# Performance work log

Hardware: AMD Instinct MI355X
Metric: run time of the kernel (lower is better)

The kernel has to match this reference:

```python
import jax, jax.numpy as jnp
import numpy as np

N, E = 10000, 320000
NF, HF = 256, 256  # input_nf/output_nf, hidden_nf
EPS = 1e-8


def setup_inputs() -> dict:
    key = jax.random.key(0)
    ks = jax.random.split(key, 20)
    h = jax.random.normal(ks[0], (N, NF), jnp.float32)
    coord = jax.random.normal(ks[1], (N, 3), jnp.float32)
    edge_index = jax.random.randint(ks[2], (2, E), 0, N, jnp.int32)

    def dense(k, fan_in, fan_out, scale=None):
        s = scale if scale is not None else 1.0 / np.sqrt(fan_in)
        W = jax.random.normal(k, (fan_in, fan_out), jnp.float32) * s
        b = jnp.zeros((fan_out,), jnp.float32)
        return W, b

    We1, be1 = dense(ks[3], 2 * NF + 1, HF)   # edge_mlp layer 1
    We2, be2 = dense(ks[4], HF, HF)           # edge_mlp layer 2
    Wn1, bn1 = dense(ks[5], HF + NF, HF)      # node_mlp layer 1
    Wn2, bn2 = dense(ks[6], HF, NF)           # node_mlp layer 2
    Wc1, bc1 = dense(ks[7], HF, HF)           # coord_mlp layer 1
    Wc2, bc2 = dense(ks[8], HF, 1, scale=0.001)  # coord_mlp final, tiny init (xavier gain=0.001)
    return dict(h=h, coord=coord, edge_index=edge_index,
                We1=We1, be1=be1, We2=We2, be2=be2,
                Wn1=Wn1, bn1=bn1, Wn2=Wn2, bn2=bn2,
                Wc1=Wc1, bc1=bc1, Wc2=Wc2, bc2=bc2)


def _segment_sum(data, seg_ids, num_segments):
    return jax.ops.segment_sum(data, seg_ids, num_segments=num_segments)


def reference(h, coord, edge_index, We1, be1, We2, be2, Wn1, bn1, Wn2, bn2, Wc1, bc1, Wc2, bc2):
    row, col = edge_index[0], edge_index[1]

    # coord2radial
    coord_diff = coord[row] - coord[col]                    # [E, 3]
    radial = jnp.sum(coord_diff ** 2, axis=1, keepdims=True)  # [E, 1]

    # edge model: MLP on [h_i, h_j, ||x_i - x_j||^2]
    edge_in = jnp.concatenate([h[row], h[col], radial], axis=1)  # [E, 2*NF+1]
    e = jax.nn.silu(edge_in @ We1 + be1)
    edge_feat = jax.nn.silu(e @ We2 + be2)                  # [E, HF]

    # coord model: coord_diff * coord_mlp(edge_feat), mean-aggregated
    c = jax.nn.silu(edge_feat @ Wc1 + bc1)
    trans = coord_diff * (c @ Wc2 + bc2)                    # [E, 3]
    agg_c = _segment_sum(trans, row, coord.shape[0])
    count = _segment_sum(jnp.ones_like(trans), row, coord.shape[0])
    coord_out = coord + agg_c / jnp.clip(count, 1.0)

    # node model: sum-aggregate edge features, concat with h, MLP
    agg_h = _segment_sum(edge_feat, row, h.shape[0])        # [N, HF]
    node_in = jnp.concatenate([h, agg_h], axis=1)           # [N, HF+NF]
    n = jax.nn.silu(node_in @ Wn1 + bn1)
    h_out = n @ Wn2 + bn2                                   # [N, NF]

    return h_out, coord_out
```

## Files before the change

kernel.cpp:

```cpp
#include <hip/hip_runtime.h>
#include <hip/hip_bf16.h>

typedef __bf16 bf16;
typedef __attribute__((ext_vector_type(8))) __bf16 bf16x8;
typedef __attribute__((ext_vector_type(4))) float f32x4;

static_assert(sizeof(bf16x8) == 16, "bf16x8 must be 16B");

constexpr int N_NODES = 10000;
constexpr int N_EDGES = 320000;
constexpr int KPAD    = 264;

__device__ __forceinline__ float rcp_f(float x) {
  float r; asm("v_rcp_f32 %0, %1" : "=v"(r) : "v"(x)); return r;
}
__device__ __forceinline__ float silu_f(float x) { return x * rcp_f(1.0f + __expf(-x)); }

__device__ __forceinline__ unsigned pk_bf16(float lo, float hi) {
  unsigned r;
  asm("v_cvt_pk_bf16_f32 %0, %1, %2" : "=v"(r) : "v"(lo), "v"(hi));
  return r;
}

__device__ __forceinline__ void mfmaT_k256(const bf16* __restrict__ WT, int wstride, int koff,
                                           const bf16* Albs, int w, int r, int q, f32x4 acc[4][4]) {
  for (int k0 = 0; k0 < 256; k0 += 32) {
    bf16x8 a[4], b[4];
#pragma unroll
    for (int mi = 0; mi < 4; ++mi)
      a[mi] = *(const bf16x8*)(WT + (size_t)(w * 64 + 16 * mi + r) * wstride + koff + k0 + q * 8);
#pragma unroll
    for (int ni = 0; ni < 4; ++ni)
      b[ni] = *(const bf16x8*)(Albs + (16 * ni + r) * KPAD + k0 + q * 8);
#pragma unroll
    for (int mi = 0; mi < 4; ++mi)
#pragma unroll
      for (int ni = 0; ni < 4; ++ni)
        acc[mi][ni] = __builtin_amdgcn_mfma_f32_16x16x32_bf16(a[mi], b[ni], acc[mi][ni], 0, 0, 0);
  }
}

__device__ __forceinline__ void mfmaT_k256_b1(const bf16* __restrict__ WT, int wstride, int koff,
                                              const bf16* Albs, int w, int r, int q, f32x4 acc[4]) {
  for (int k0 = 0; k0 < 256; k0 += 32) {
    bf16x8 a[4], b;
    b = *(const bf16x8*)(Albs + r * KPAD + k0 + q * 8);
#pragma unroll
    for (int mi = 0; mi < 4; ++mi)
      a[mi] = *(const bf16x8*)(WT + (size_t)(w * 64 + 16 * mi + r) * wstride + koff + k0 + q * 8);
#pragma unroll
    for (int mi = 0; mi < 4; ++mi)
      acc[mi] = __builtin_amdgcn_mfma_f32_16x16x32_bf16(a[mi], b, acc[mi], 0, 0, 0);
  }
}

__device__ __forceinline__ void transpose512(const float* __restrict__ W, bf16* __restrict__ WT,
                                             int local, int tid) {
  int tg = local * 256 + tid;
  int j = tg >> 6, k0 = (tg & 63) * 8;
  bf16x8 v;
#pragma unroll
  for (int i = 0; i < 8; ++i) v[i] = (bf16)W[(size_t)(k0 + i) * 256 + j];
  *(bf16x8*)(WT + (size_t)j * 512 + k0) = v;
}
__device__ __forceinline__ void transpose256(const float* __restrict__ W, bf16* __restrict__ WT,
                                             int local, int tid) {
  int tg = local * 256 + tid;
  int j = tg >> 5, k0 = (tg & 31) * 8;
  bf16x8 v;
#pragma unroll
  for (int i = 0; i < 8; ++i) v[i] = (bf16)W[(size_t)(k0 + i) * 256 + j];
  *(bf16x8*)(WT + (size_t)j * 256 + k0) = v;
}

__global__ __launch_bounds__(256) void prep_kernel(
    const float* __restrict__ h, const float* __restrict__ We1, const float* __restrict__ We2,
    const float* __restrict__ Wn1, const float* __restrict__ Wn2, const float* __restrict__ Wc1,
    const int* __restrict__ eidx,
    bf16* __restrict__ Hb, bf16* __restrict__ We1T, bf16* __restrict__ Wn1T,
    bf16* __restrict__ We2T, bf16* __restrict__ Wn2T, bf16* __restrict__ Wc1T,
    int* __restrict__ hist, float4* __restrict__ zero_base) {
  int bid = blockIdx.x, tid = threadIdx.x;
  if (bid < 10000) { int i = bid * 256 + tid; Hb[i] = (bf16)h[i]; return; }
  if (bid < 10224) {
    int wb = bid - 10000;
    if (wb < 64)       transpose512(We1, We1T, wb, tid);
    else if (wb < 128) transpose512(Wn1, Wn1T, wb - 64, tid);
    else if (wb < 160) transpose256(We2, We2T, wb - 128, tid);
    else if (wb < 192) transpose256(Wn2, Wn2T, wb - 160, tid);
    else               transpose256(Wc1, Wc1T, wb - 192, tid);
    return;
  }
  if (bid < 11474) {
    int e = (bid - 11474 + 1250) * 256 + tid - 1250 * 256;
    e = (bid - 10224) * 256 + tid;
    if (e < N_EDGES) atomicAdd(&hist[eidx[e]], 1);
    return;
  }
  int z = (bid - 11474) * 256 + tid;
  if (z < 647500) zero_base[z] = (float4){0.f, 0.f, 0.f, 0.f};
}

__global__ __launch_bounds__(256) void scan_kernel(const int* __restrict__ hist,
                                                   int* __restrict__ base, int* __restrict__ cursor) {
  __shared__ int sh[10000];
  __shared__ int partial[256];
  int t = threadIdx.x;
  for (int i = 0; i < 40; ++i) { int idx = i * 256 + t; if (idx < N_NODES) sh[idx] = hist[idx]; }
  __syncthreads();
  int s = 0;
  for (int i = 0; i < 40; ++i) { int idx = t * 40 + i; if (idx < N_NODES) s += sh[idx]; }
  partial[t] = s;
  __syncthreads();
  for (int d = 1; d < 256; d <<= 1) {
    int v = (t >= d) ? partial[t - d] : 0;
    __syncthreads();
    partial[t] += v;
    __syncthreads();
  }
  int run = partial[t] - s;
  for (int i = 0; i < 40; ++i) {
    int idx = t * 40 + i;
    if (idx < N_NODES) { int hv = sh[idx]; sh[idx] = run; run += hv; }
  }
  __syncthreads();
  for (int i = 0; i < 40; ++i) {
    int idx = i * 256 + t;
    if (idx < N_NODES) { int v = sh[idx]; base[idx] = v; cursor[idx] = v; }
  }
}

__global__ __launch_bounds__(256) void scatter_kernel(const int* __restrict__ eidx, int* __restrict__ cursor,
                                                      int2* __restrict__ rc) {
  int e = blockIdx.x * 256 + threadIdx.x;
  if (e < N_EDGES) {
    int r = eidx[e], c = eidx[N_EDGES + e];
    int p = atomicAdd(&cursor[r], 1);
    rc[p] = (int2){r, c};
  }
}

__global__ __launch_bounds__(256, 2) void gemm_pq(const bf16* __restrict__ Hb,
                                                  const bf16* __restrict__ We1T,
                                                  const float* __restrict__ be1,
                                                  bf16* __restrict__ P, bf16* __restrict__ Q) {
  int tid = threadIdx.x, w = tid >> 6, lane = tid & 63, r = lane & 15, q = lane >> 4;
  int m0 = blockIdx.x * 16;
  int koff = blockIdx.y ? 256 : 0;
  bf16* OUT = blockIdx.y ? Q : P;
  bool addb = (blockIdx.y == 0);
  f32x4 acc[4];
#pragma unroll
  for (int mi = 0; mi < 4; ++mi) acc[mi] = (f32x4){0.f, 0.f, 0.f, 0.f};
  int m = m0 + r;

  for (int k0 = 0; k0 < 256; k0 += 32) {
    bf16x8 a[4], b;
    b = *(const bf16x8*)(Hb + (size_t)m * 256 + k0 + q * 8);
#pragma unroll
    for (int mi = 0; mi < 4; ++mi)
      a[mi] = *(const bf16x8*)(We1T + (size_t)(w * 64 + 16 * mi + r) * 512 + koff + k0 + q * 8);
#pragma unroll
    for (int mi = 0; mi < 4; ++mi)
      acc[mi] = __builtin_amdgcn_mfma_f32_16x16x32_bf16(a[mi], b, acc[mi], 0, 0, 0);
  }
#pragma unroll
  for (int mi = 0; mi < 4; ++mi) {
    int ch = w * 64 + 16 * mi + 4 * q;
    float4 bv = addb ? *(const float4*)(be1 + ch) : (float4){0.f, 0.f, 0.f, 0.f};
    uint2 o;
    o.x = pk_bf16(acc[mi][0] + bv.x, acc[mi][1] + bv.y);
    o.y = pk_bf16(acc[mi][2] + bv.z, acc[mi][3] + bv.w);
    *(uint2*)(OUT + (size_t)m * 256 + ch) = o;
  }
}

__global__ __launch_bounds__(256, 4) void edge_kernel(
    const float* __restrict__ coord, const int2* __restrict__ rc,
    const float* __restrict__ We1,
    const float* __restrict__ be2, const float* __restrict__ bc1,
    const float* __restrict__ Wc2, const float* __restrict__ bc2,
    const bf16* __restrict__ P, const bf16* __restrict__ Q,
    const bf16* __restrict__ We2T, const bf16* __restrict__ Wc1T,
    float* __restrict__ agg_h, float* __restrict__ agg_c) {
  __shared__ __align__(16) bf16 buf[64 * KPAD];
  __shared__ int s_row[64], s_col[64];
  __shared__ float s_rad[64], s_cd[64][3], s_part[64][4], s_scal[64];
  __shared__ int s_rs[65];
  __shared__ int s_nrun;

  int tid = threadIdx.x;
  int e0 = blockIdx.x * 64;
  int w = tid >> 6, lane = tid & 63, r = lane & 15, q = lane >> 4;

  if (tid < 64) {
    int2 v = rc[e0 + tid];
    int ri = v.x, ci = v.y;
    s_row[tid] = ri; s_col[tid] = ci;
    float dx = coord[3 * ri + 0] - coord[3 * ci + 0];
    float dy = coord[3 * ri + 1] - coord[3 * ci + 1];
    float dz = coord[3 * ri + 2] - coord[3 * ci + 2];
    s_cd[tid][0] = dx; s_cd[tid][1] = dy; s_cd[tid][2] = dz;
    s_rad[tid] = dx * dx + dy * dy + dz * dz;
  }
  __syncthreads();

  if (tid < 64) {
    bool bnd = (tid == 0) || (s_row[tid] != s_row[tid - 1]);
    unsigned long long m = __ballot(bnd);
    int rank = __popcll(m & ((1ull << tid) - 1ull));
    if (bnd) s_rs[rank] = tid;
    if (tid == 0) { int R = __popcll(m); s_nrun = R; s_rs[R] = 64; }
  }

  {
    int off = (tid & 31) * 8;
    int esub = tid >> 5;
    float4 wa = *(const float4*)(We1 + 512 * 256 + off);
    float4 wb = *(const float4*)(We1 + 512 * 256 + off + 4);
#pragma unroll
    for (int p = 0; p < 8; ++p) {
      int e = p * 8 + esub;
      int ri = s_row[e], ci = s_col[e];
      bf16x8 pv = *(const bf16x8*)(P + (size_t)ri * 256 + off);
      bf16x8 qv = *(const bf16x8*)(Q + (size_t)ci * 256 + off);
      float rad = s_rad[e];
      float f0 = silu_f((float)pv[0] + (float)qv[0] + rad * wa.x);
      float f1 = silu_f((float)pv[1] + (float)qv[1] + rad * wa.y);
      float f2 = silu_f((float)pv[2] + (float)qv[2] + rad * wa.z);
      float f3 = silu_f((float)pv[3] + (float)qv[3] + rad * wa.w);
      float f4 = silu_f((float)pv[4] + (float)qv[4] + rad * wb.x);
      float f5 = silu_f((float)pv[5] + (float)qv[5] + rad * wb.y);
      float f6 = silu_f((float)pv[6] + (float)qv[6] + rad * wb.z);
      float f7 = silu_f((float)pv[7] + (float)qv[7] + rad * wb.w);
      uint4 o;
      o.x = pk_bf16(f0, f1); o.y = pk_bf16(f2, f3);
      o.z = pk_bf16(f4, f5); o.w = pk_bf16(f6, f7);
      *(uint4*)(buf + e * KPAD + off) = o;
    }
  }
  __syncthreads();

  {
    f32x4 acc[4][4];
#pragma unroll
    for (int mi = 0; mi < 4; ++mi)
#pragma unroll
      for (int ni = 0; ni < 4; ++ni) acc[mi][ni] = (f32x4){0.f, 0.f, 0.f, 0.f};
    mfmaT_k256(We2T, 256, 0, buf, w, r, q, acc);
    __syncthreads();
#pragma unroll
    for (int mi = 0; mi < 4; ++mi) {
      int ch = w * 64 + 16 * mi + 4 * q;
      float4 bv = *(const float4*)(be2 + ch);
#pragma unroll
      for (int ni = 0; ni < 4; ++ni) {
        int edge = 16 * ni + r;
        float f0 = silu_f(acc[mi][ni][0] + bv.x);
        float f1 = silu_f(acc[mi][ni][1] + bv.y);
        float f2 = silu_f(acc[mi][ni][2] + bv.z);
        float f3 = silu_f(acc[mi][ni][3] + bv.w);
        uint2 o; o.x = pk_bf16(f0, f1); o.y = pk_bf16(f2, f3);
        *(uint2*)(buf + edge * KPAD + ch) = o;
      }
    }
  }
  __syncthreads();

  f32x4 acc2[4][4];
#pragma unroll
  for (int mi = 0; mi < 4; ++mi)
#pragma unroll
    for (int ni = 0; ni < 4; ++ni) acc2[mi][ni] = (f32x4){0.f, 0.f, 0.f, 0.f};
  mfmaT_k256(Wc1T, 256, 0, buf, w, r, q, acc2);

  {
    int R = s_nrun;
    for (int rr = 0; rr < R; ++rr) {
      int st = s_rs[rr], en = s_rs[rr + 1];
      float s = 0.f;
      for (int e = st; e < en; ++e) s += (float)buf[e * KPAD + tid];
      atomicAdd(&agg_h[(size_t)s_row[st] * 256 + tid], s);
    }
  }

  {
    float p[4] = {0.f, 0.f, 0.f, 0.f};
#pragma unroll
    for (int mi = 0; mi < 4; ++mi) {
      int ch = w * 64 + 16 * mi + 4 * q;
      float4 bv = *(const float4*)(bc1 + ch);
      float4 wv = *(const float4*)(Wc2 + ch);
#pragma unroll
      for (int ni = 0; ni < 4; ++ni) {
        p[ni] += silu_f(acc2[mi][ni][0] + bv.x) * wv.x
               + silu_f(acc2[mi][ni][1] + bv.y) * wv.y
               + silu_f(acc2[mi][ni][2] + bv.z) * wv.z
               + silu_f(acc2[mi][ni][3] + bv.w) * wv.w;
      }
    }
#pragma unroll
    for (int ni = 0; ni < 4; ++ni) {
      float v = p[ni];
      v += __shfl_xor(v, 16, 64);
      v += __shfl_xor(v, 32, 64);
      if (q == 0) s_part[16 * ni + r][w] = v;
    }
  }
  __syncthreads();

  if (tid < 64)
    s_scal[tid] = s_part[tid][0] + s_part[tid][1] + s_part[tid][2] + s_part[tid][3] + bc2[0];
  __syncthreads();

  if (tid < 3) {
    int R = s_nrun;
    for (int rr = 0; rr < R; ++rr) {
      int st = s_rs[rr], en = s_rs[rr + 1];
      float s = 0.f;
      for (int e = st; e < en; ++e) s += s_cd[e][tid] * s_scal[e];
      atomicAdd(&agg_c[3 * s_row[st] + tid], s);
    }
  }
}

__global__ __launch_bounds__(256, 2) void node_kernel(
    const bf16* __restrict__ Hb, const float* __restrict__ agg_h,
    const int* __restrict__ hist, const float* __restrict__ coord, const float* __restrict__ agg_c,
    const bf16* __restrict__ Wn1T, const bf16* __restrict__ Wn2T,
    const float* __restrict__ bn1, const float* __restrict__ bn2,
    float* __restrict__ h_out, float* __restrict__ coord_out) {
  __shared__ __align__(16) bf16 buf[16 * KPAD];
  int tid = threadIdx.x, w = tid >> 6, lane = tid & 63, r = lane & 15, q = lane >> 4;
  int m0 = blockIdx.x * 16;
  int m = m0 + r;

  if (tid < 16) {
    int mm = m0 + tid;
    float c = (float)hist[mm]; if (c < 1.f) c = 1.f;
    coord_out[3 * mm + 0] = coord[3 * mm + 0] + agg_c[3 * mm + 0] / c;
    coord_out[3 * mm + 1] = coord[3 * mm + 1] + agg_c[3 * mm + 1] / c;
    coord_out[3 * mm + 2] = coord[3 * mm + 2] + agg_c[3 * mm + 2] / c;
  }

  f32x4 acc[4];
#pragma unroll
  for (int mi = 0; mi < 4; ++mi) acc[mi] = (f32x4){0.f, 0.f, 0.f, 0.f};
  for (int k0 = 0; k0 < 256; k0 += 32) {
    bf16x8 a[4], b;
    b = *(const bf16x8*)(Hb + (size_t)m * 256 + k0 + q * 8);
#pragma unroll
    for (int mi = 0; mi < 4; ++mi)
      a[mi] = *(const bf16x8*)(Wn1T + (size_t)(w * 64 + 16 * mi + r) * 512 + k0 + q * 8);
#pragma unroll
    for (int mi = 0; mi < 4; ++mi)
      acc[mi] = __builtin_amdgcn_mfma_f32_16x16x32_bf16(a[mi], b, acc[mi], 0, 0, 0);
  }
  for (int k0 = 0; k0 < 256; k0 += 32) {
    bf16x8 a[4], b;
    {
      const float* ap = agg_h + (size_t)m * 256 + k0 + q * 8;
      float4 u = *(const float4*)ap;
      float4 v = *(const float4*)(ap + 4);
      uint4 o;
      o.x = pk_bf16(u.x, u.y); o.y = pk_bf16(u.z, u.w);
      o.z = pk_bf16(v.x, v.y); o.w = pk_bf16(v.z, v.w);
      b = *(const bf16x8*)&o;
    }
#pragma unroll
    for (int mi = 0; mi < 4; ++mi)
      a[mi] = *(const bf16x8*)(Wn1T + (size_t)(w * 64 + 16 * mi + r) * 512 + 256 + k0 + q * 8);
#pragma unroll
    for (int mi = 0; mi < 4; ++mi)
      acc[mi] = __builtin_amdgcn_mfma_f32_16x16x32_bf16(a[mi], b, acc[mi], 0, 0, 0);
  }
  __syncthreads();
#pragma unroll
  for (int mi = 0; mi < 4; ++mi) {
    int ch = w * 64 + 16 * mi + 4 * q;
    float4 bv = *(const float4*)(bn1 + ch);
    float f0 = silu_f(acc[mi][0] + bv.x);
    float f1 = silu_f(acc[mi][1] + bv.y);
    float f2 = silu_f(acc[mi][2] + bv.z);
    float f3 = silu_f(acc[mi][3] + bv.w);
    uint2 o; o.x = pk_bf16(f0, f1); o.y = pk_bf16(f2, f3);
    *(uint2*)(buf + r * KPAD + ch) = o;
  }
  __syncthreads();
  f32x4 acc2[4];
#pragma unroll
  for (int mi = 0; mi < 4; ++mi) acc2[mi] = (f32x4){0.f, 0.f, 0.f, 0.f};
  mfmaT_k256_b1(Wn2T, 256, 0, buf, w, r, q, acc2);
#pragma unroll
  for (int mi = 0; mi < 4; ++mi) {
    int ch = w * 64 + 16 * mi + 4 * q;
    float4 bv = *(const float4*)(bn2 + ch);
    float4 o;
    o.x = acc2[mi][0] + bv.x;
    o.y = acc2[mi][1] + bv.y;
    o.z = acc2[mi][2] + bv.z;
    o.w = acc2[mi][3] + bv.w;
    *(float4*)(h_out + (size_t)m * 256 + ch) = o;
  }
}

extern "C" void kernel_launch(void* const* d_in, const int* in_sizes, int n_in,
                              void* d_out, int out_size, void* d_ws, size_t ws_size,
                              hipStream_t stream) {
  const float* h     = (const float*)d_in[0];
  const float* coord = (const float*)d_in[1];
  const int*   eidx  = (const int*)d_in[2];
  const float* We1 = (const float*)d_in[3];
  const float* be1 = (const float*)d_in[4];
  const float* We2 = (const float*)d_in[5];
  const float* be2 = (const float*)d_in[6];
  const float* Wn1 = (const float*)d_in[7];
  const float* bn1 = (const float*)d_in[8];
  const float* Wn2 = (const float*)d_in[9];
  const float* bn2 = (const float*)d_in[10];
  const float* Wc1 = (const float*)d_in[11];
  const float* bc1 = (const float*)d_in[12];
  const float* Wc2 = (const float*)d_in[13];
  const float* bc2 = (const float*)d_in[14];

  char* ws = (char*)d_ws;
  float* agg_h = (float*)(ws + 0);
  float* agg_c = (float*)(ws + 10240000);
  int*   hist  = (int*)  (ws + 10360000);
  int*   base  = (int*)  (ws + 10400000);
  int*   cursor= (int*)  (ws + 10440000);
  int2*  rc    = (int2*) (ws + 10480000);
  bf16* Hb   = (bf16*)(ws + 13040000);
  bf16* P    = (bf16*)(ws + 18160000);
  bf16* Q    = (bf16*)(ws + 23280000);
  bf16* We1T = (bf16*)(ws + 28400000);
  bf16* Wn1T = (bf16*)(ws + 28662144);
  bf16* We2T = (bf16*)(ws + 28924288);
  bf16* Wn2T = (bf16*)(ws + 29055360);
  bf16* Wc1T = (bf16*)(ws + 29186432);

  float* h_out = (float*)d_out;
  float* coord_out = h_out + (size_t)N_NODES * 256;

  hipMemsetAsync(hist, 0, 40000, stream);
  prep_kernel<<<14014, 256, 0, stream>>>(h, We1, We2, Wn1, Wn2, Wc1, eidx,
                                         Hb, We1T, Wn1T, We2T, Wn2T, Wc1T, hist,
                                         (float4*)agg_h);
  scan_kernel<<<1, 256, 0, stream>>>(hist, base, cursor);
  scatter_kernel<<<1250, 256, 0, stream>>>(eidx, cursor, rc);
  gemm_pq<<<dim3(625, 2), 256, 0, stream>>>(Hb, We1T, be1, P, Q);
  edge_kernel<<<5000, 256, 0, stream>>>(coord, rc, We1, be2, bc1, Wc2, bc2,
                                        P, Q, We2T, Wc1T, agg_h, agg_c);
  node_kernel<<<625, 256, 0, stream>>>(Hb, agg_h, hist, coord, agg_c,
                                       Wn1T, Wn2T, bn1, bn2, h_out, coord_out);
}
```

Measured before the change: 409.0 us.

## Merge scatter with P/Q GEMM, prefetch gathers, parallelize edge aggregation atomics

Measured after the change: 544.4 us. +33.1%, slower.

```diff
diff --git a/kernel.cpp b/kernel.cpp
--- a/kernel.cpp
+++ b/kernel.cpp
@@ -3,9 +3,11 @@
 
 typedef __bf16 bf16;
 typedef __attribute__((ext_vector_type(8))) __bf16 bf16x8;
+typedef __attribute__((ext_vector_type(4))) __bf16 bf16x4;
 typedef __attribute__((ext_vector_type(4))) float f32x4;
 
 static_assert(sizeof(bf16x8) == 16, "bf16x8 must be 16B");
+static_assert(sizeof(bf16x4) == 8, "bf16x4 must be 8B");
 
 constexpr int N_NODES = 10000;
 constexpr int N_EDGES = 320000;
@@ -92,8 +94,7 @@
     return;
   }
   if (bid < 11474) {
-    int e = (bid - 11474 + 1250) * 256 + tid - 1250 * 256;
-    e = (bid - 10224) * 256 + tid;
+    int e = (bid - 10224) * 256 + tid;
     if (e < N_EDGES) atomicAdd(&hist[eidx[e]], 1);
     return;
   }
@@ -101,54 +102,55 @@
   if (z < 647500) zero_base[z] = (float4){0.f, 0.f, 0.f, 0.f};
 }
 
-__global__ __launch_bounds__(256) void scan_kernel(const int* __restrict__ hist,
-                                                   int* __restrict__ base, int* __restrict__ cursor) {
+__global__ __launch_bounds__(1024) void scan_kernel(const int* __restrict__ hist,
+                                                    int* __restrict__ cursor) {
   __shared__ int sh[10000];
-  __shared__ int partial[256];
+  __shared__ int partial[1024];
   int t = threadIdx.x;
-  for (int i = 0; i < 40; ++i) { int idx = i * 256 + t; if (idx < N_NODES) sh[idx] = hist[idx]; }
+  for (int i = 0; i < 10; ++i) { int idx = i * 1024 + t; if (idx < N_NODES) sh[idx] = hist[idx]; }
   __syncthreads();
   int s = 0;
-  for (int i = 0; i < 40; ++i) { int idx = t * 40 + i; if (idx < N_NODES) s += sh[idx]; }
+  for (int i = 0; i < 10; ++i) { int idx = t * 10 + i; if (idx < N_NODES) s += sh[idx]; }
   partial[t] = s;
   __syncthreads();
-  for (int d = 1; d < 256; d <<= 1) {
+  for (int d = 1; d < 1024; d <<= 1) {
     int v = (t >= d) ? partial[t - d] : 0;
     __syncthreads();
     partial[t] += v;
     __syncthreads();
   }
   int run = partial[t] - s;
-  for (int i = 0; i < 40; ++i) {
-    int idx = t * 40 + i;
+  for (int i = 0; i < 10; ++i) {
+    int idx = t * 10 + i;
     if (idx < N_NODES) { int hv = sh[idx]; sh[idx] = run; run += hv; }
   }
   __syncthreads();
-  for (int i = 0; i < 40; ++i) {
-    int idx = i * 256 + t;
-    if (idx < N_NODES) { int v = sh[idx]; base[idx] = v; cursor[idx] = v; }
-  }
-}
-
-__global__ __launch_bounds__(256) void scatter_kernel(const int* __restrict__ eidx, int* __restrict__ cursor,
-                                                      int2* __restrict__ rc) {
-  int e = blockIdx.x * 256 + threadIdx.x;
-  if (e < N_EDGES) {
-    int r = eidx[e], c = eidx[N_EDGES + e];
-    int p = atomicAdd(&cursor[r], 1);
-    rc[p] = (int2){r, c};
-  }
-}
-
-__global__ __launch_bounds__(256, 2) void gemm_pq(const bf16* __restrict__ Hb,
-                                                  const bf16* __restrict__ We1T,
-                                                  const float* __restrict__ be1,
-                                                  bf16* __restrict__ P, bf16* __restrict__ Q) {
-  int tid = threadIdx.x, w = tid >> 6, lane = tid & 63, r = lane & 15, q = lane >> 4;
-  int m0 = blockIdx.x * 16;
-  int koff = blockIdx.y ? 256 : 0;
-  bf16* OUT = blockIdx.y ? Q : P;
-  bool addb = (blockIdx.y == 0);
+  for (int i = 0; i < 10; ++i) {
+    int idx = i * 1024 + t;
+    if (idx < N_NODES) cursor[idx] = sh[idx];
+  }
+}
+
+__global__ __launch_bounds__(256, 4) void scatter_gemm(
+    const int* __restrict__ eidx, int* __restrict__ cursor, int2* __restrict__ rc,
+    const bf16* __restrict__ Hb, const bf16* __restrict__ We1T,
+    const float* __restrict__ be1, bf16* __restrict__ P, bf16* __restrict__ Q) {
+  int bid = blockIdx.x, tid = threadIdx.x;
+  if (bid < 1250) {
+    int e = bid * 256 + tid;
+    if (e < N_EDGES) {
+      int r = eidx[e], c = eidx[N_EDGES + e];
+      int p = atomicAdd(&cursor[r], 1);
+      rc[p] = (int2){r, c};
+    }
+    return;
+  }
+  int g = bid - 1250;
+  int w = tid >> 6, lane = tid & 63, r = lane & 15, q = lane >> 4;
+  int m0 = (g >> 1) * 16;
+  int koff = (g & 1) ? 256 : 0;
+  bf16* OUT = (g & 1) ? Q : P;
+  bool addb = !(g & 1);
   f32x4 acc[4];
 #pragma unroll
   for (int mi = 0; mi < 4; ++mi) acc[mi] = (f32x4){0.f, 0.f, 0.f, 0.f};
@@ -184,7 +186,7 @@
     const bf16* __restrict__ We2T, const bf16* __restrict__ Wc1T,
     float* __restrict__ agg_h, float* __restrict__ agg_c) {
   __shared__ __align__(16) bf16 buf[64 * KPAD];
-  __shared__ int s_row[64], s_col[64];
+  __shared__ int s_row[64];
   __shared__ float s_rad[64], s_cd[64][3], s_part[64][4], s_scal[64];
   __shared__ int s_rs[65];
   __shared__ int s_nrun;
@@ -193,10 +195,19 @@
   int e0 = blockIdx.x * 64;
   int w = tid >> 6, lane = tid & 63, r = lane & 15, q = lane >> 4;
 
+  int offv = (tid & 31) * 8;
+  int esub = tid >> 5;
+  int2 rc0 = rc[e0 + esub];
+  bf16x8 pv = *(const bf16x8*)(P + (size_t)rc0.x * 256 + offv);
+  bf16x8 qv = *(const bf16x8*)(Q + (size_t)rc0.y * 256 + offv);
+  int2 rcn = rc[e0 + 8 + esub];
+  float4 wa = *(const float4*)(We1 + 512 * 256 + offv);
+  float4 wb = *(const float4*)(We1 + 512 * 256 + offv + 4);
+
   if (tid < 64) {
     int2 v = rc[e0 + tid];
     int ri = v.x, ci = v.y;
-    s_row[tid] = ri; s_col[tid] = ci;
+    s_row[tid] = ri;
     float dx = coord[3 * ri + 0] - coord[3 * ci + 0];
     float dy = coord[3 * ri + 1] - coord[3 * ci + 1];
     float dz = coord[3 * ri + 2] - coord[3 * ci + 2];
@@ -213,31 +224,28 @@
     if (tid == 0) { int R = __popcll(m); s_nrun = R; s_rs[R] = 64; }
   }
 
-  {
-    int off = (tid & 31) * 8;
-    int esub = tid >> 5;
-    float4 wa = *(const float4*)(We1 + 512 * 256 + off);
-    float4 wb = *(const float4*)(We1 + 512 * 256 + off + 4);
-#pragma unroll
-    for (int p = 0; p < 8; ++p) {
-      int e = p * 8 + esub;
-      int ri = s_row[e], ci = s_col[e];
-      bf16x8 pv = *(const bf16x8*)(P + (size_t)ri * 256 + off);
-      bf16x8 qv = *(const bf16x8*)(Q + (size_t)ci * 256 + off);
-      float rad = s_rad[e];
-      float f0 = silu_f((float)pv[0] + (float)qv[0] + rad * wa.x);
-      float f1 = silu_f((float)pv[1] + (float)qv[1] + rad * wa.y);
-      float f2 = silu_f((float)pv[2] + (float)qv[2] + rad * wa.z);
-      float f3 = silu_f((float)pv[3] + (float)qv[3] + rad * wa.w);
-      float f4 = silu_f((float)pv[4] + (float)qv[4] + rad * wb.x);
-      float f5 = silu_f((float)pv[5] + (float)qv[5] + rad * wb.y);
-      float f6 = silu_f((float)pv[6] + (float)qv[6] + rad * wb.z);
-      float f7 = silu_f((float)pv[7] + (float)qv[7] + rad * wb.w);
-      uint4 o;
-      o.x = pk_bf16(f0, f1); o.y = pk_bf16(f2, f3);
-      o.z = pk_bf16(f4, f5); o.w = pk_bf16(f6, f7);
-      *(uint4*)(buf + e * KPAD + off) = o;
-    }
+#pragma unroll
+  for (int p = 0; p < 8; ++p) {
+    bf16x8 pvc = pv, qvc = qv;
+    if (p < 7) {
+      pv = *(const bf16x8*)(P + (size_t)rcn.x * 256 + offv);
+      qv = *(const bf16x8*)(Q + (size_t)rcn.y * 256 + offv);
+    }
+    if (p < 6) rcn = rc[e0 + (p + 2) * 8 + esub];
+    int e = p * 8 + esub;
+    float rad = s_rad[e];
+    float f0 = silu_f((float)pvc[0] + (float)qvc[0] + rad * wa.x);
+    float f1 = silu_f((float)pvc[1] + (float)qvc[1] + rad * wa.y);
+    float f2 = silu_f((float)pvc[2] + (float)qvc[2] + rad * wa.z);
+    float f3 = silu_f((float)pvc[3] + (float)qvc[3] + rad * wa.w);
+    float f4 = silu_f((float)pvc[4] + (float)qvc[4] + rad * wb.x);
+    float f5 = silu_f((float)pvc[5] + (float)qvc[5] + rad * wb.y);
+    float f6 = silu_f((float)pvc[6] + (float)qvc[6] + rad * wb.z);
+    float f7 = silu_f((float)pvc[7] + (float)qvc[7] + rad * wb.w);
+    uint4 o;
+    o.x = pk_bf16(f0, f1); o.y = pk_bf16(f2, f3);
+    o.z = pk_bf16(f4, f5); o.w = pk_bf16(f6, f7);
+    *(uint4*)(buf + e * KPAD + offv) = o;
   }
   __syncthreads();
 
@@ -276,11 +284,21 @@
 
   {
     int R = s_nrun;
+    int qq = tid >> 6, cg = tid & 63;
     for (int rr = 0; rr < R; ++rr) {
       int st = s_rs[rr], en = s_rs[rr + 1];
-      float s = 0.f;
-      for (int e = st; e < en; ++e) s += (float)buf[e * KPAD + tid];
-      atomicAdd(&agg_h[(size_t)s_row[st] * 256 + tid], s);
+      int lo = st > 16 * qq ? st : 16 * qq;
+      int hi = en < 16 * qq + 16 ? en : 16 * qq + 16;
+      if (lo < hi) {
+        float s0 = 0.f, s1 = 0.f, s2 = 0.f, s3 = 0.f;
+        for (int e = lo; e < hi; ++e) {
+          bf16x4 v = *(const bf16x4*)(buf + e * KPAD + 4 * cg);
+          s0 += (float)v[0]; s1 += (float)v[1]; s2 += (float)v[2]; s3 += (float)v[3];
+        }
+        float* dst = agg_h + (size_t)s_row[lo] * 256 + 4 * cg;
+        atomicAdd(dst + 0, s0); atomicAdd(dst + 1, s1);
+        atomicAdd(dst + 2, s2); atomicAdd(dst + 3, s3);
+      }
     }
   }
 
@@ -313,14 +331,10 @@
     s_scal[tid] = s_part[tid][0] + s_part[tid][1] + s_part[tid][2] + s_part[tid][3] + bc2[0];
   __syncthreads();
 
-  if (tid < 3) {
-    int R = s_nrun;
-    for (int rr = 0; rr < R; ++rr) {
-      int st = s_rs[rr], en = s_rs[rr + 1];
-      float s = 0.f;
-      for (int e = st; e < en; ++e) s += s_cd[e][tid] * s_scal[e];
-      atomicAdd(&agg_c[3 * s_row[st] + tid], s);
-    }
+  {
+    int comp = tid >> 6, e = tid & 63;
+    if (comp < 3)
+      atomicAdd(&agg_c[3 * s_row[e] + comp], s_cd[e][comp] * s_scal[e]);
   }
 }
 
@@ -427,7 +441,6 @@
   float* agg_h = (float*)(ws + 0);
   float* agg_c = (float*)(ws + 10240000);
   int*   hist  = (int*)  (ws + 10360000);
-  int*   base  = (int*)  (ws + 10400000);
   int*   cursor= (int*)  (ws + 10440000);
   int2*  rc    = (int2*) (ws + 10480000);
   bf16* Hb   = (bf16*)(ws + 13040000);
@@ -446,9 +459,8 @@
   prep_kernel<<<14014, 256, 0, stream>>>(h, We1, We2, Wn1, Wn2, Wc1, eidx,
                                          Hb, We1T, Wn1T, We2T, Wn2T, Wc1T, hist,
                                          (float4*)agg_h);
-  scan_kernel<<<1, 256, 0, stream>>>(hist, base, cursor);
-  scatter_kernel<<<1250, 256, 0, stream>>>(eidx, cursor, rc);
-  gemm_pq<<<dim3(625, 2), 256, 0, stream>>>(Hb, We1T, be1, P, Q);
+  scan_kernel<<<1, 1024, 0, stream>>>(hist, cursor);
+  scatter_gemm<<<2500, 256, 0, stream>>>(eidx, cursor, rc, Hb, We1T, be1, P, Q);
   edge_kernel<<<5000, 256, 0, stream>>>(coord, rc, We1, be2, bc1, Wc2, bc2,
                                         P, Q, We2T, Wc1T, agg_h, agg_c);
   node_kernel<<<625, 256, 0, stream>>>(Hb, agg_h, hist, coord, agg_c,
```
